# Kernel tuning notes

Measured on AMD Instinct MI355X. Metric: run time of the kernel, lower is better.

The kernel has to match this reference:

```python
import jax, jax.numpy as jnp
import numpy as np

N_NODES = 50000
N_EDGES = 600000
N_GRAPHS = 500


def gcn_conv(x, src, dst, W, b, n_nodes):
    # PyG GCNConv: add self-loops, symmetric normalization D^-1/2 (A+I) D^-1/2, then XW + b
    h = x @ W  # [N, F_out]
    loop = jnp.arange(n_nodes)
    s = jnp.concatenate([src, loop])
    d = jnp.concatenate([dst, loop])
    deg = jax.ops.segment_sum(jnp.ones_like(d, dtype=h.dtype), d, num_segments=n_nodes)
    dinv = jnp.where(deg > 0, jax.lax.rsqrt(jnp.maximum(deg, 1.0)), 0.0)
    norm = dinv[s] * dinv[d]  # [E+N]
    msg = h[s] * norm[:, None]  # gather + scale
    out = jax.ops.segment_sum(msg, d, num_segments=n_nodes)  # scatter-add
    return out + b


def setup_inputs() -> dict:
    key = jax.random.key(0)
    ks = jax.random.split(key, 12)
    F_in, H, Hf, D_out = 128, 128, 64, 1
    x = jax.random.normal(ks[0], (N_NODES, F_in), dtype=jnp.float32)
    edge_index = jax.random.randint(ks[1], (2, N_EDGES), 0, N_NODES, dtype=jnp.int64)
    batch = jnp.sort(jax.random.randint(ks[2], (N_NODES,), 0, N_GRAPHS, dtype=jnp.int64))
    def glorot(k, shape):
        lim = np.sqrt(6.0 / (shape[0] + shape[1]))
        return jax.random.uniform(k, shape, jnp.float32, -lim, lim)
    return {
        "x": x, "edge_index": edge_index, "batch": batch,
        "W1": glorot(ks[3], (F_in, H)), "b1": jnp.zeros((H,), jnp.float32),
        "W2": glorot(ks[4], (H, H)), "b2": jnp.zeros((H,), jnp.float32),
        "W3": glorot(ks[5], (H, H)), "b3": jnp.zeros((H,), jnp.float32),
        "Wf1": glorot(ks[6], (H, Hf)), "bf1": jnp.zeros((Hf,), jnp.float32),
        "Wf2": glorot(ks[7], (Hf, D_out)), "bf2": jnp.zeros((D_out,), jnp.float32),
    }


def reference(x, edge_index, batch, W1, b1, W2, b2, W3, b3, Wf1, bf1, Wf2, bf2):
    src, dst = edge_index[0], edge_index[1]
    n = x.shape[0]
    h = jax.nn.relu(gcn_conv(x, src, dst, W1, b1, n))
    h = jax.nn.relu(gcn_conv(h, src, dst, W2, b2, n))
    h = jax.nn.relu(gcn_conv(h, src, dst, W3, b3, n))
    # global_mean_pool: segment mean over graphs
    sums = jax.ops.segment_sum(h, batch, num_segments=N_GRAPHS)
    cnts = jax.ops.segment_sum(jnp.ones((n,), h.dtype), batch, num_segments=N_GRAPHS)
    hg = sums / jnp.maximum(cnts, 1.0)[:, None]  # [G, 128]
    h = jax.nn.relu(hg @ Wf1 + bf1)
    return h @ Wf2 + bf2
```

## Files before the change

### kernel.cpp

```cpp
#include <hip/hip_runtime.h>

#define N_NODES 50000
#define N_EDGES 600000
#define N_GRAPHS 500
#define F 128

typedef short bf16x8 __attribute__((ext_vector_type(8)));
typedef float f32x4 __attribute__((ext_vector_type(4)));
union U4H8 { uint4 u; bf16x8 h; };

__device__ inline unsigned pk_bf16(float a, float b) {
    unsigned ua = __float_as_uint(a), ub = __float_as_uint(b);
    ua = (ua + 0x7fffu + ((ua >> 16) & 1u)) >> 16;
    ub = (ub + 0x7fffu + ((ub >> 16) & 1u)) >> 16;
    return ua | (ub << 16);
}
__device__ inline float bf16_rnd(float x) {
    unsigned u = __float_as_uint(x);
    u = (u + 0x7fffu + ((u >> 16) & 1u)) & 0xffff0000u;
    return __uint_as_float(u);
}
__device__ inline unsigned short bf16_1(float a) {
    unsigned ua = __float_as_uint(a);
    return (unsigned short)((ua + 0x7fffu + ((ua >> 16) & 1u)) >> 16);
}
#define BF_LO(u) __uint_as_float((u) << 16)
#define BF_HI(u) __uint_as_float((u) & 0xffff0000u)

#define G_CVT  3125
#define G_HIST 2344
#define G_PREPW 24

__global__ __launch_bounds__(256) void k_prep(const float* __restrict__ x, unsigned short* __restrict__ xb,
                                              const int* __restrict__ dst, int* __restrict__ cnt,
                                              const float* __restrict__ W1, const float* __restrict__ W2,
                                              const float* __restrict__ W3,
                                              uint4* __restrict__ Whi, uint4* __restrict__ Wlo) {
    int b = blockIdx.x, tid = threadIdx.x;
    if (b < G_CVT) {
        int idx = b * 256 + tid;
        if (idx < N_NODES * F / 8) {
            const float4* xr = (const float4*)(x + (size_t)idx * 8);
            float4 a = xr[0], c = xr[1];
            uint4 o;
            o.x = pk_bf16(a.x, a.y); o.y = pk_bf16(a.z, a.w);
            o.z = pk_bf16(c.x, c.y); o.w = pk_bf16(c.z, c.w);
            ((uint4*)xb)[idx] = o;
        }
    } else if (b < G_CVT + G_HIST) {
        int e = (b - G_CVT) * 256 + tid;
        if (e < N_EDGES) atomicAdd(&cnt[dst[e]], 1);
    } else {
        int idx = (b - G_CVT - G_HIST) * 256 + tid;
        int layer = idx >> 11;
        const float* W = (layer == 0) ? W1 : (layer == 1) ? W2 : W3;
        int t = idx & 2047;
        int lane = t & 63, sc = t >> 6;
        int s = sc >> 3, c = sc & 7;
        int q = lane >> 4, m = lane & 15;
        int k0 = 32 * s + 8 * q, n0 = 16 * c + m;
        float w[8], h[8];
        #pragma unroll
        for (int j = 0; j < 8; ++j) {
            w[j] = W[(k0 + j) * F + n0];
            h[j] = bf16_rnd(w[j]);
        }
        uint4 uh, ul;
        uh.x = pk_bf16(h[0], h[1]); uh.y = pk_bf16(h[2], h[3]);
        uh.z = pk_bf16(h[4], h[5]); uh.w = pk_bf16(h[6], h[7]);
        ul.x = pk_bf16(w[0] - h[0], w[1] - h[1]); ul.y = pk_bf16(w[2] - h[2], w[3] - h[3]);
        ul.z = pk_bf16(w[4] - h[4], w[5] - h[5]); ul.w = pk_bf16(w[6] - h[6], w[7] - h[7]);
        Whi[idx] = uh;
        Wlo[idx] = ul;
    }
}

__global__ __launch_bounds__(256) void k_scan1(const int* __restrict__ cnt, int* __restrict__ row_ptr,
                                               int* __restrict__ blksums, float* __restrict__ dinv, int n) {
    __shared__ int s[256];
    int i = blockIdx.x * 256 + threadIdx.x;
    int v = (i < n) ? cnt[i] : 0;
    if (i < n) dinv[i] = rsqrtf((float)(v + 1));
    s[threadIdx.x] = v;
    __syncthreads();
    for (int off = 1; off < 256; off <<= 1) {
        int t = (threadIdx.x >= off) ? s[threadIdx.x - off] : 0;
        __syncthreads();
        s[threadIdx.x] += t;
        __syncthreads();
    }
    if (i < n) row_ptr[i] = s[threadIdx.x] - v;
    if (threadIdx.x == 255) blksums[blockIdx.x] = s[255];
}

__global__ __launch_bounds__(256) void k_scan23(int* __restrict__ row_ptr, const int* __restrict__ blksums,
                                                int n, int ne) {
    __shared__ int s[256];
    int tid = threadIdx.x;
    s[tid] = (tid < (int)blockIdx.x) ? blksums[tid] : 0;
    __syncthreads();
    for (int off = 128; off > 0; off >>= 1) {
        if (tid < off) s[tid] += s[tid + off];
        __syncthreads();
    }
    int base = s[0];
    int i = blockIdx.x * 256 + tid;
    if (i < n) row_ptr[i] += base;
    if (i == 0) row_ptr[n] = ne;
}

__global__ __launch_bounds__(256) void k_fill(const int* __restrict__ src, const int* __restrict__ dst,
                                              const int* __restrict__ row_ptr, int* __restrict__ cnt,
                                              const float* __restrict__ dinv,
                                              int2* __restrict__ esw, int ne) {
    int e = blockIdx.x * 256 + threadIdx.x;
    if (e < ne) {
        int d = dst[e];
        int s = src[e];
        int pos = row_ptr[d] + atomicSub(&cnt[d], 1) - 1;
        esw[pos] = make_int2(s, __float_as_int(dinv[s]));
    }
}

#define TN 32
#define GP2 136
#define MAXE_L 1024
__global__ __launch_bounds__(256) void k_fused(const int* __restrict__ row_ptr,
                                               const int2* __restrict__ esw,
                                               const float* __restrict__ dinv,
                                               const unsigned short* __restrict__ Hin,
                                               const uint4* __restrict__ Whi,
                                               const uint4* __restrict__ Wlo,
                                               const float* __restrict__ bias,
                                               unsigned short* __restrict__ Hout, int n) {
    __shared__ unsigned short Gb[TN * GP2];
    __shared__ uint2 eL[MAXE_L];
    __shared__ int rp[TN + 1];
    __shared__ float ddl[TN];
    int tid = threadIdx.x;
    int d0 = blockIdx.x * TN;

    int dTN = d0 + TN; if (dTN > n) dTN = n;
    int e0 = row_ptr[d0];
    int e1 = row_ptr[dTN];
    if (tid <= TN) {
        int d = d0 + tid; if (d > n) d = n;
        rp[tid] = row_ptr[d];
    }
    if (tid < TN) {
        int d = d0 + tid;
        ddl[tid] = (d < n) ? dinv[d] : 0.f;
    }
    int nE = e1 - e0; if (nE > MAXE_L) nE = MAXE_L;
    for (int i = tid; i < nE; i += 256) eL[i] = ((const uint2*)esw)[e0 + i];
    __syncthreads();

    int grp = tid >> 4, sub = tid & 15;

    #pragma unroll
    for (int i = 0; i < 2; ++i) {
        int nl = 2 * grp + i;
        int node = d0 + nl;
        float4 accL = make_float4(0.f, 0.f, 0.f, 0.f);
        float4 accH = make_float4(0.f, 0.f, 0.f, 0.f);
        if (node < n) {
            int beg = rp[nl], end = rp[nl + 1];
            float dd = ddl[nl];
            uint4 srow = ((const uint4*)(Hin + (size_t)node * F))[sub];
            float ws = dd * dd;
            accL.x = BF_LO(srow.x) * ws;
            accL.y = BF_HI(srow.x) * ws;
            accL.z = BF_LO(srow.y) * ws;
            accL.w = BF_HI(srow.y) * ws;
            accH.x = BF_LO(srow.z) * ws;
            accH.y = BF_HI(srow.z) * ws;
            accH.z = BF_LO(srow.w) * ws;
            accH.w = BF_HI(srow.w) * ws;
            for (int c = beg; c < end; c += 8) {
                int sjs[8];
                #pragma unroll
                for (int j = 0; j < 8; ++j) {
                    int e = c + j;
                    int sj = node;
                    if (e < end) {
                        int off = e - e0;
                        sj = (off < MAXE_L) ? (int)((const unsigned*)eL)[2 * off]
                                            : ((const uint2*)esw)[e].x;
                    }
                    sjs[j] = sj;
                }
                uint4 rows[8];
                #pragma unroll
                for (int j = 0; j < 8; ++j)
                    rows[j] = ((const uint4*)(Hin + (size_t)sjs[j] * F))[sub];
                #pragma unroll
                for (int j = 0; j < 8; ++j) {
                    int e = c + j;
                    float wj = 0.f;
                    if (e < end) {
                        int off = e - e0;
                        unsigned wb = (off < MAXE_L) ? ((const unsigned*)eL)[2 * off + 1]
                                                     : (unsigned)((const uint2*)esw)[e].y;
                        wj = __uint_as_float(wb) * dd;
                    }
                    accL.x = fmaf(BF_LO(rows[j].x), wj, accL.x);
                    accL.y = fmaf(BF_HI(rows[j].x), wj, accL.y);
                    accL.z = fmaf(BF_LO(rows[j].y), wj, accL.z);
                    accL.w = fmaf(BF_HI(rows[j].y), wj, accL.w);
                    accH.x = fmaf(BF_LO(rows[j].z), wj, accH.x);
                    accH.y = fmaf(BF_HI(rows[j].z), wj, accH.y);
                    accH.z = fmaf(BF_LO(rows[j].w), wj, accH.z);
                    accH.w = fmaf(BF_HI(rows[j].w), wj, accH.w);
                }
            }
        }
        uint4 o;
        o.x = pk_bf16(accL.x, accL.y);
        o.y = pk_bf16(accL.z, accL.w);
        o.z = pk_bf16(accH.x, accH.y);
        o.w = pk_bf16(accH.z, accH.w);
        *(uint4*)&Gb[nl * GP2 + 8 * sub] = o;
    }
    __syncthreads();

    int wave = tid >> 6, lane = tid & 63;
    int q = lane >> 4, m = lane & 15;
    int rt = wave & 1;
    int ch = (wave >> 1) * 4;
    int row0 = 16 * rt;
    f32x4 acc[4];
    #pragma unroll
    for (int c = 0; c < 4; ++c) acc[c] = (f32x4){0.f, 0.f, 0.f, 0.f};
    #pragma unroll
    for (int s = 0; s < 4; ++s) {
        U4H8 a;
        a.u = *(const uint4*)&Gb[(row0 + m) * GP2 + 32 * s + 8 * q];
        #pragma unroll
        for (int cc = 0; cc < 4; ++cc) {
            int c = ch + cc;
            U4H8 bh, bl;
            bh.u = Whi[(s * 8 + c) * 64 + lane];
            bl.u = Wlo[(s * 8 + c) * 64 + lane];
            acc[cc] = __builtin_amdgcn_mfma_f32_16x16x32_bf16(a.h, bh.h, acc[cc], 0, 0, 0);
            acc[cc] = __builtin_amdgcn_mfma_f32_16x16x32_bf16(a.h, bl.h, acc[cc], 0, 0, 0);
        }
    }
    __syncthreads();

    #pragma unroll
    for (int cc = 0; cc < 4; ++cc) {
        int c = ch + cc;
        float bb = bias[16 * c + m];
        #pragma unroll
        for (int r = 0; r < 4; ++r)
            Gb[(row0 + 4 * q + r) * GP2 + 16 * c + m] = bf16_1(fmaxf(acc[cc][r] + bb, 0.f));
    }
    __syncthreads();
    #pragma unroll
    for (int j = 0; j < 2; ++j) {
        int lin = tid + 256 * j;
        int row = lin >> 4, c8 = lin & 15;
        int node = d0 + row;
        if (node < n) {
            uint4 o = *(const uint4*)&Gb[row * GP2 + c8 * 8];
            ((uint4*)(Hout + (size_t)node * F))[c8] = o;
        }
    }
}

__global__ __launch_bounds__(256) void k_pool_fc(const unsigned short* __restrict__ Hb,
                                                 const int* __restrict__ batch,
                                                 const float* __restrict__ Wf1,
                                                 const float* __restrict__ bf1,
                                                 const float* __restrict__ Wf2,
                                                 const float* __restrict__ bf2,
                                                 float* __restrict__ out) {
    int g = blockIdx.x;
    int tid = threadIdx.x;
    int lo = 0, hi = N_NODES;
    while (lo < hi) { int mid = (lo + hi) >> 1; if (batch[mid] < g) lo = mid + 1; else hi = mid; }
    int start = lo;
    hi = N_NODES;
    while (lo < hi) { int mid = (lo + hi) >> 1; if (batch[mid] <= g) lo = mid + 1; else hi = mid; }
    int end = lo;

    __shared__ float hs[4][F];
    __shared__ float hg[F];
    int wv = tid >> 6, lane = tid & 63;
    int half = lane >> 5, sub = lane & 31;
    float4 a = make_float4(0.f, 0.f, 0.f, 0.f);
    for (int i = start + wv * 2 + half; i < end; i += 8) {
        uint2 v = ((const uint2*)(Hb + (size_t)i * F))[sub];
        a.x += BF_LO(v.x); a.y += BF_HI(v.x);
        a.z += BF_LO(v.y); a.w += BF_HI(v.y);
    }
    a.x += __shfl_xor(a.x, 32, 64);
    a.y += __shfl_xor(a.y, 32, 64);
    a.z += __shfl_xor(a.z, 32, 64);
    a.w += __shfl_xor(a.w, 32, 64);
    if (half == 0) ((float4*)hs[wv])[sub] = a;
    __syncthreads();
    if (tid < F) {
        float inv = 1.0f / (float)((end - start) > 0 ? (end - start) : 1);
        hg[tid] = (hs[0][tid] + hs[1][tid] + hs[2][tid] + hs[3][tid]) * inv;
    }
    __syncthreads();
    if (tid < 64) {
        float acc = bf1[tid];
        #pragma unroll 4
        for (int f = 0; f < F; ++f) acc = fmaf(hg[f], Wf1[f * 64 + tid], acc);
        float v = fmaxf(acc, 0.f) * Wf2[tid];
        #pragma unroll
        for (int off = 32; off > 0; off >>= 1) v += __shfl_down(v, off, 64);
        if (tid == 0) out[g] = v + bf2[0];
    }
}

extern "C" void kernel_launch(void* const* d_in, const int* in_sizes, int n_in,
                              void* d_out, int out_size, void* d_ws, size_t ws_size,
                              hipStream_t stream) {
    const float* x    = (const float*)d_in[0];
    const int* eidx   = (const int*)d_in[1];
    const int* batch  = (const int*)d_in[2];
    const float* W1   = (const float*)d_in[3];
    const float* b1   = (const float*)d_in[4];
    const float* W2   = (const float*)d_in[5];
    const float* b2   = (const float*)d_in[6];
    const float* W3   = (const float*)d_in[7];
    const float* b3   = (const float*)d_in[8];
    const float* Wf1  = (const float*)d_in[9];
    const float* bf1  = (const float*)d_in[10];
    const float* Wf2  = (const float*)d_in[11];
    const float* bf2  = (const float*)d_in[12];
    float* out = (float*)d_out;

    const int* src = eidx;
    const int* dst = eidx + N_EDGES;

    char* p = (char*)d_ws;
    unsigned short* Xb  = (unsigned short*)p;  p += (size_t)N_NODES * F * 2;
    unsigned short* H1  = (unsigned short*)p;  p += (size_t)N_NODES * F * 2;
    unsigned short* H2  = (unsigned short*)p;  p += (size_t)N_NODES * F * 2;
    unsigned short* H3  = (unsigned short*)p;  p += (size_t)N_NODES * F * 2;
    int2* esw   = (int2*)p;    p += (size_t)N_EDGES * sizeof(int2);
    uint4* Whi  = (uint4*)p;   p += (size_t)3 * 2048 * sizeof(uint4);
    uint4* Wlo  = (uint4*)p;   p += (size_t)3 * 2048 * sizeof(uint4);
    float* dinv = (float*)p;   p += (size_t)N_NODES * sizeof(float);
    int* cnt     = (int*)p;    p += (size_t)N_NODES * sizeof(int);
    int* row_ptr = (int*)p;    p += (size_t)(N_NODES + 1) * sizeof(int);
    int* blksums = (int*)p;    p += 256 * sizeof(int);

    dim3 b256(256);
    int gNodes = (N_NODES + 255) / 256;
    int gEdges = (N_EDGES + 255) / 256;
    int gFused = (N_NODES + TN - 1) / TN;

    hipMemsetAsync(cnt, 0, (size_t)N_NODES * sizeof(int), stream);
    k_prep<<<G_CVT + G_HIST + G_PREPW, b256, 0, stream>>>(x, Xb, dst, cnt, W1, W2, W3, Whi, Wlo);

    k_scan1<<<gNodes, b256, 0, stream>>>(cnt, row_ptr, blksums, dinv, N_NODES);
    k_scan23<<<gNodes, b256, 0, stream>>>(row_ptr, blksums, N_NODES, N_EDGES);
    k_fill<<<gEdges, b256, 0, stream>>>(src, dst, row_ptr, cnt, dinv, esw, N_EDGES);

    k_fused<<<gFused, b256, 0, stream>>>(row_ptr, esw, dinv, Xb, Whi,        Wlo,        b1, H1, N_NODES);
    k_fused<<<gFused, b256, 0, stream>>>(row_ptr, esw, dinv, H1, Whi + 2048, Wlo + 2048, b2, H2, N_NODES);
    k_fused<<<gFused, b256, 0, stream>>>(row_ptr, esw, dinv, H2, Whi + 4096, Wlo + 4096, b3, H3, N_NODES);

    k_pool_fc<<<N_GRAPHS, b256, 0, stream>>>(H3, batch, Wf1, bf1, Wf2, bf2, out);
}
```

Before: 272.9 us.

## Gather neighbor rows via global_load_lds into per-wave LDS buffers with smaller node tiles

The fused aggregate-and-GEMM kernel now processes 16 nodes per block instead of 32. Each wave handles four destination nodes, issuing up to 16 neighbor-row gathers per batch as direct global-to-LDS loads, then reducing two features per lane. The self-loop is folded into the edge loop as an extra entry. This is meant to raise occupancy and memory-level parallelism for the irregular gather. In exchange it adds a full waitcnt stall per batch and LDS round trips, uses narrow 4-byte loads per lane, and leaves each wave doing half as much MFMA work.

New measurement: 340.6 us. 24.8% more time.

```diff
diff --git a/kernel.cpp b/kernel.cpp
--- a/kernel.cpp
+++ b/kernel.cpp
@@ -122,9 +122,9 @@
     }
 }
 
-#define TN 32
+#define TN 16
 #define GP2 136
-#define MAXE_L 1024
+#define CAPE 768
 __global__ __launch_bounds__(256) void k_fused(const int* __restrict__ row_ptr,
                                                const int2* __restrict__ esw,
                                                const float* __restrict__ dinv,
@@ -134,10 +134,12 @@
                                                const float* __restrict__ bias,
                                                unsigned short* __restrict__ Hout, int n) {
     __shared__ unsigned short Gb[TN * GP2];
-    __shared__ uint2 eL[MAXE_L];
+    __shared__ uint2 eL[CAPE];
+    __shared__ unsigned short rowbuf[4][16][128];
     __shared__ int rp[TN + 1];
     __shared__ float ddl[TN];
     int tid = threadIdx.x;
+    int wave = tid >> 6, lane = tid & 63;
     int d0 = blockIdx.x * TN;
 
     int dTN = d0 + TN; if (dTN > n) dTN = n;
@@ -151,93 +153,77 @@
         int d = d0 + tid;
         ddl[tid] = (d < n) ? dinv[d] : 0.f;
     }
-    int nE = e1 - e0; if (nE > MAXE_L) nE = MAXE_L;
+    int nE = e1 - e0; if (nE > CAPE) nE = CAPE;
     for (int i = tid; i < nE; i += 256) eL[i] = ((const uint2*)esw)[e0 + i];
     __syncthreads();
 
-    int grp = tid >> 4, sub = tid & 15;
-
-    #pragma unroll
-    for (int i = 0; i < 2; ++i) {
-        int nl = 2 * grp + i;
+    for (int k = 0; k < 4; ++k) {
+        int nl = wave * 4 + k;
         int node = d0 + nl;
-        float4 accL = make_float4(0.f, 0.f, 0.f, 0.f);
-        float4 accH = make_float4(0.f, 0.f, 0.f, 0.f);
+        float a0 = 0.f, a1 = 0.f;
         if (node < n) {
             int beg = rp[nl], end = rp[nl + 1];
             float dd = ddl[nl];
-            uint4 srow = ((const uint4*)(Hin + (size_t)node * F))[sub];
-            float ws = dd * dd;
-            accL.x = BF_LO(srow.x) * ws;
-            accL.y = BF_HI(srow.x) * ws;
-            accL.z = BF_LO(srow.y) * ws;
-            accL.w = BF_HI(srow.y) * ws;
-            accH.x = BF_LO(srow.z) * ws;
-            accH.y = BF_HI(srow.z) * ws;
-            accH.z = BF_LO(srow.w) * ws;
-            accH.w = BF_HI(srow.w) * ws;
-            for (int c = beg; c < end; c += 8) {
-                int sjs[8];
+            for (int c = beg; c <= end; c += 16) {
+                int ns = end - c + 1; if (ns > 16) ns = 16;
+                int rows[16];
                 #pragma unroll
-                for (int j = 0; j < 8; ++j) {
-                    int e = c + j;
-                    int sj = node;
-                    if (e < end) {
-                        int off = e - e0;
-                        sj = (off < MAXE_L) ? (int)((const unsigned*)eL)[2 * off]
-                                            : ((const uint2*)esw)[e].x;
+                for (int j = 0; j < 16; ++j) {
+                    if (j < ns) {
+                        int e = c + j;
+                        if (e == end) rows[j] = node;
+                        else {
+                            int off = e - e0;
+                            rows[j] = (off < CAPE) ? (int)eL[off].x
+                                                   : (int)((const uint2*)esw)[e].x;
+                        }
                     }
-                    sjs[j] = sj;
                 }
-                uint4 rows[8];
                 #pragma unroll
-                for (int j = 0; j < 8; ++j)
-                    rows[j] = ((const uint4*)(Hin + (size_t)sjs[j] * F))[sub];
+                for (int j = 0; j < 16; ++j) {
+                    if (j < ns) {
+                        const unsigned* gp = (const unsigned*)(Hin + (size_t)rows[j] * F) + lane;
+                        __builtin_amdgcn_global_load_lds(
+                            (const __attribute__((address_space(1))) unsigned*)gp,
+                            (__attribute__((address_space(3))) unsigned*)&rowbuf[wave][j][0],
+                            4, 0, 0);
+                    }
+                }
+                __builtin_amdgcn_s_waitcnt(0);
                 #pragma unroll
-                for (int j = 0; j < 8; ++j) {
-                    int e = c + j;
-                    float wj = 0.f;
-                    if (e < end) {
-                        int off = e - e0;
-                        unsigned wb = (off < MAXE_L) ? ((const unsigned*)eL)[2 * off + 1]
-                                                     : (unsigned)((const uint2*)esw)[e].y;
-                        wj = __uint_as_float(wb) * dd;
+                for (int j = 0; j < 16; ++j) {
+                    if (j < ns) {
+                        int e = c + j;
+                        float w;
+                        if (e == end) w = dd * dd;
+                        else {
+                            int off = e - e0;
+                            unsigned wy = (off < CAPE) ? eL[off].y
+                                                       : (unsigned)((const uint2*)esw)[e].y;
+                            w = __uint_as_float(wy) * dd;
+                        }
+                        unsigned v = *(const unsigned*)&rowbuf[wave][j][lane * 2];
+                        a0 = fmaf(BF_LO(v), w, a0);
+                        a1 = fmaf(BF_HI(v), w, a1);
                     }
-                    accL.x = fmaf(BF_LO(rows[j].x), wj, accL.x);
-                    accL.y = fmaf(BF_HI(rows[j].x), wj, accL.y);
-                    accL.z = fmaf(BF_LO(rows[j].y), wj, accL.z);
-                    accL.w = fmaf(BF_HI(rows[j].y), wj, accL.w);
-                    accH.x = fmaf(BF_LO(rows[j].z), wj, accH.x);
-                    accH.y = fmaf(BF_HI(rows[j].z), wj, accH.y);
-                    accH.z = fmaf(BF_LO(rows[j].w), wj, accH.z);
-                    accH.w = fmaf(BF_HI(rows[j].w), wj, accH.w);
                 }
             }
         }
-        uint4 o;
-        o.x = pk_bf16(accL.x, accL.y);
-        o.y = pk_bf16(accL.z, accL.w);
-        o.z = pk_bf16(accH.x, accH.y);
-        o.w = pk_bf16(accH.z, accH.w);
-        *(uint4*)&Gb[nl * GP2 + 8 * sub] = o;
-    }
-    __syncthreads();
-
-    int wave = tid >> 6, lane = tid & 63;
+        *(unsigned*)&Gb[nl * GP2 + lane * 2] = (node < n) ? pk_bf16(a0, a1) : 0u;
+    }
+    __syncthreads();
+
     int q = lane >> 4, m = lane & 15;
-    int rt = wave & 1;
-    int ch = (wave >> 1) * 4;
-    int row0 = 16 * rt;
-    f32x4 acc[4];
-    #pragma unroll
-    for (int c = 0; c < 4; ++c) acc[c] = (f32x4){0.f, 0.f, 0.f, 0.f};
+    f32x4 acc[2];
+    acc[0] = (f32x4){0.f, 0.f, 0.f, 0.f};
+    acc[1] = (f32x4){0.f, 0.f, 0.f, 0.f};
     #pragma unroll
     for (int s = 0; s < 4; ++s) {
         U4H8 a;
-        a.u = *(const uint4*)&Gb[(row0 + m) * GP2 + 32 * s + 8 * q];
+        a.u = *(const uint4*)&Gb[m * GP2 + 32 * s + 8 * q];
         #pragma unroll
-        for (int cc = 0; cc < 4; ++cc) {
-            int c = ch + cc;
+        for (int cc = 0; cc < 2; ++cc) {
+            int c = wave * 2 + cc;
             U4H8 bh, bl;
             bh.u = Whi[(s * 8 + c) * 64 + lane];
             bl.u = Wlo[(s * 8 + c) * 64 + lane];
@@ -248,18 +234,16 @@
     __syncthreads();
 
     #pragma unroll
-    for (int cc = 0; cc < 4; ++cc) {
-        int c = ch + cc;
+    for (int cc = 0; cc < 2; ++cc) {
+        int c = wave * 2 + cc;
         float bb = bias[16 * c + m];
         #pragma unroll
         for (int r = 0; r < 4; ++r)
-            Gb[(row0 + 4 * q + r) * GP2 + 16 * c + m] = bf16_1(fmaxf(acc[cc][r] + bb, 0.f));
-    }
-    __syncthreads();
-    #pragma unroll
-    for (int j = 0; j < 2; ++j) {
-        int lin = tid + 256 * j;
-        int row = lin >> 4, c8 = lin & 15;
+            Gb[(4 * q + r) * GP2 + 16 * c + m] = bf16_1(fmaxf(acc[cc][r] + bb, 0.f));
+    }
+    __syncthreads();
+    {
+        int row = tid >> 4, c8 = tid & 15;
         int node = d0 + row;
         if (node < n) {
             uint4 o = *(const uint4*)&Gb[row * GP2 + c8 * 8];
```
